# Performance work log

Hardware: AMD Instinct MI355X
Metric: run time of the kernel (lower is better)

The kernel has to match this reference:

```python
import jax, jax.numpy as jnp
import numpy as np

D_MODEL = 1024
H = 16
D_K = D_MODEL // H
B, S = 4, 2048


def setup_inputs() -> dict:
    key = jax.random.key(0)
    ks = jax.random.split(key, 12)
    s = 1.0 / np.sqrt(D_MODEL)
    inp = {
        "q": jax.random.normal(ks[0], (B, S, D_MODEL), jnp.float32),
        "k": jax.random.normal(ks[1], (B, S, D_MODEL), jnp.float32),
        "v": jax.random.normal(ks[2], (B, S, D_MODEL), jnp.float32),
        "mask": jax.random.randint(ks[3], (1, 1, S, S), 0, 2, jnp.int32),
        # torch nn.Linear convention: weight [out, in], y = x @ W.T + b
        "w_q": jax.random.uniform(ks[4], (D_MODEL, D_MODEL), jnp.float32, -s, s),
        "b_q": jax.random.uniform(ks[5], (D_MODEL,), jnp.float32, -s, s),
        "w_k": jax.random.uniform(ks[6], (D_MODEL, D_MODEL), jnp.float32, -s, s),
        "b_k": jax.random.uniform(ks[7], (D_MODEL,), jnp.float32, -s, s),
        "w_v": jax.random.uniform(ks[8], (D_MODEL, D_MODEL), jnp.float32, -s, s),
        "b_v": jax.random.uniform(ks[9], (D_MODEL,), jnp.float32, -s, s),
        "w_o": jax.random.uniform(ks[10], (D_MODEL, D_MODEL), jnp.float32, -s, s),
        "b_o": jax.random.uniform(ks[11], (D_MODEL,), jnp.float32, -s, s),
    }
    return inp


def _split_heads(x):
    b, s, _ = x.shape
    return x.reshape(b, s, H, D_K).transpose(0, 2, 1, 3)  # [B,H,S,Dk]


def reference(q, k, v, mask, w_q, b_q, w_k, b_k, w_v, b_v, w_o, b_o):
    query = _split_heads(q @ w_q.T + b_q)
    key = _split_heads(k @ w_k.T + b_k)
    value = _split_heads(v @ w_v.T + b_v)
    scores = jnp.einsum("bhqd,bhkd->bhqk", query, key) / jnp.sqrt(
        jnp.asarray(D_K, query.dtype))
    scores = jnp.where(mask == 0, jnp.asarray(-1e9, scores.dtype), scores)
    attn = jax.nn.softmax(scores, axis=-1)  # dropout p=0 (eval) -> identity
    x = jnp.einsum("bhqk,bhkd->bhqd", attn, value)
    x = x.transpose(0, 2, 1, 3).reshape(q.shape[0], -1, H * D_K)
    return x @ w_o.T + b_o
```

## Files before the change

### kernel.cpp

```cpp
#include <hip/hip_runtime.h>

typedef __bf16 bf16_t;
typedef __bf16 bf16x4 __attribute__((ext_vector_type(4)));
typedef __bf16 bf16x8 __attribute__((ext_vector_type(8)));
typedef float f32x4 __attribute__((ext_vector_type(4)));
typedef float f32x16 __attribute__((ext_vector_type(16)));
typedef unsigned int uint;
typedef uint uint2v __attribute__((ext_vector_type(2)));
typedef uint uint4v __attribute__((ext_vector_type(4)));

#define CSCALE 0.18033688011112042f

static __device__ __forceinline__ bf16_t f2bf(float f) {
  unsigned u = __builtin_bit_cast(unsigned, f);
  u = (u + 0x7fff + ((u >> 16) & 1)) >> 16;
  unsigned short h = (unsigned short)u;
  return __builtin_bit_cast(bf16_t, h);
}
static __device__ __forceinline__ uint cvt_pk(float a, float b) {
  uint r;
  asm("v_cvt_pk_bf16_f32 %0, %1, %2" : "=v"(r) : "v"(a), "v"(b));
  return r;
}

#define GLD_LDS(g, l) \
  __builtin_amdgcn_global_load_lds((const __attribute__((address_space(1))) void*)(g), \
                                   (__attribute__((address_space(3))) void*)(l), 16, 0, 0)
#define VMCNT(n) asm volatile("s_waitcnt vmcnt(" #n ")" ::: "memory")
#define LGKM0() asm volatile("s_waitcnt lgkmcnt(0)" ::: "memory")
#define BARRIER() do { __builtin_amdgcn_s_barrier(); __builtin_amdgcn_sched_barrier(0); } while (0)

__global__ void cvt4_f2b(const float* __restrict__ a, const float* __restrict__ b,
                         const float* __restrict__ c, const float* __restrict__ d,
                         bf16_t* __restrict__ oa, bf16_t* __restrict__ ob,
                         bf16_t* __restrict__ oc, bf16_t* __restrict__ od) {
  int i = blockIdx.x * 256 + threadIdx.x;
  const float* src = a;
  bf16_t* dst = oa;
  int w = i >> 18;
  i &= 262143;
  if (w == 1) { src = b; dst = ob; }
  else if (w == 2) { src = c; dst = oc; }
  else if (w == 3) { src = d; dst = od; }
  const float4 f = reinterpret_cast<const float4*>(src)[i];
  bf16x4 o;
  o[0] = f2bf(f.x); o[1] = f2bf(f.y); o[2] = f2bf(f.z); o[3] = f2bf(f.w);
  reinterpret_cast<bf16x4*>(dst)[i] = o;
}

__global__ void mask_bits_k(const int* __restrict__ m, uint* __restrict__ out) {
  int i = blockIdx.x * 256 + threadIdx.x;
  int q = i & 2047, t = i >> 11;
  const int* mrow = m + (size_t)q * 2048 + t * 32;
  uint bits = 0;
#pragma unroll
  for (int j = 0; j < 16; ++j) {
    int r0 = (j & 3) + 8 * (j >> 2);
    bits |= (mrow[r0] ? 1u : 0u) << j;
    bits |= (mrow[r0 + 4] ? 1u : 0u) << (16 + j);
  }
  out[(size_t)t * 2048 + q] = bits;
}

__global__ __launch_bounds__(256, 2) void qkv_gemm(
    const float* __restrict__ qA, const float* __restrict__ kA, const float* __restrict__ vA,
    const bf16_t* __restrict__ wq, const bf16_t* __restrict__ wk, const bf16_t* __restrict__ wv,
    const float* __restrict__ bq, const float* __restrict__ bk, const float* __restrict__ bv,
    bf16_t* __restrict__ Qp, bf16_t* __restrict__ Kp, bf16_t* __restrict__ Vt) {
  constexpr int K = 1024;
  __shared__ __align__(16) bf16_t AsB[2][128 * 32];
  __shared__ __align__(16) bf16_t BsB[3][256 * 32];
  const int z = blockIdx.z;
  const float* A = (z == 0) ? qA : (z == 1) ? kA : vA;
  const bf16_t* W = (z == 0) ? wq : (z == 1) ? wk : wv;
  const float* bias = (z == 0) ? bq : (z == 1) ? bk : bv;

  const int tid = threadIdx.x;
  const int lane = tid & 63;
  const int wv_ = tid >> 6;
  const int wm = (wv_ & 1) * 64, wn = (wv_ >> 1) * 128;
  const int l15 = lane & 15, lhi = lane >> 4;
  const int bm = blockIdx.x, bn = blockIdx.y;

  const int arow0 = tid >> 3;
  const int acol = tid & 7;
  const float* gA = A + (size_t)(bm * 128 + arow0) * K + acol * 4;
  const int brows = tid >> 2;
  const bf16_t* gB = W + (size_t)(bn * 256 + brows) * K + ((tid & 3) ^ (brows & 3)) * 8;

  f32x4 acc[4][8] = {};
  f32x4 rA0[4], rA1[4];

  auto A_LOAD = [&](int t, f32x4* R) {
#pragma unroll
    for (int L = 0; L < 4; ++L)
      R[L] = *reinterpret_cast<const f32x4*>(gA + (size_t)L * 32 * K + t * 32);
  };
  auto A_WRITE = [&](const f32x4* R, int buf) {
#pragma unroll
    for (int L = 0; L < 4; ++L) {
      int row = arow0 + L * 32;
      uint2v u;
      u[0] = cvt_pk(R[L][0], R[L][1]);
      u[1] = cvt_pk(R[L][2], R[L][3]);
      char* p = (char*)&AsB[buf][0] + row * 64 + (((acol >> 1) ^ (row & 3)) * 16) + (acol & 1) * 8;
      *reinterpret_cast<uint2v*>(p) = u;
    }
  };
  auto B_STAGE = [&](int t, int buf) {
#pragma unroll
    for (int c2 = 0; c2 < 4; ++c2)
      GLD_LDS(gB + (size_t)c2 * 64 * K + t * 32, (char*)&BsB[buf][0] + c2 * 4096 + wv_ * 1024);
  };
  auto COMPUTE = [&](int ba, int bb) {
    bf16x8 af[4], bfv[8];
#pragma unroll
    for (int i = 0; i < 4; ++i) {
      int arow = wm + i * 16 + l15;
      af[i] = *reinterpret_cast<const bf16x8*>(
          (const char*)&AsB[ba][0] + arow * 64 + ((lhi ^ (arow & 3)) * 16));
    }
#pragma unroll
    for (int j = 0; j < 8; ++j) {
      int br = wn + j * 16 + l15;
      bfv[j] = *reinterpret_cast<const bf16x8*>(
          (const char*)&BsB[bb][0] + br * 64 + ((lhi ^ (br & 3)) * 16));
    }
#pragma unroll
    for (int i = 0; i < 4; ++i)
#pragma unroll
      for (int j = 0; j < 8; ++j)
        acc[i][j] = __builtin_amdgcn_mfma_f32_16x16x32_bf16(af[i], bfv[j], acc[i][j], 0, 0, 0);
  };

#define QSTEP(T, RL, RW, BAW, BAC, BBC, BBS) \
  A_LOAD((T) + 2, RL); B_STAGE((T) + 2, BBS); \
  COMPUTE(BAC, BBC); \
  VMCNT(8); \
  A_WRITE(RW, BAW); \
  LGKM0(); BARRIER();

  A_LOAD(0, rA0); B_STAGE(0, 0);
  A_LOAD(1, rA1); B_STAGE(1, 1);
  VMCNT(8);
  A_WRITE(rA0, 0);
  LGKM0(); BARRIER();

#pragma unroll 1
  for (int t6 = 0; t6 < 30; t6 += 6) {
    QSTEP(t6 + 0, rA0, rA1, 1, 0, 0, 2)
    QSTEP(t6 + 1, rA1, rA0, 0, 1, 1, 0)
    QSTEP(t6 + 2, rA0, rA1, 1, 0, 2, 1)
    QSTEP(t6 + 3, rA1, rA0, 0, 1, 0, 2)
    QSTEP(t6 + 4, rA0, rA1, 1, 0, 1, 0)
    QSTEP(t6 + 5, rA1, rA0, 0, 1, 2, 1)
  }
  COMPUTE(0, 0);
  VMCNT(4);
  A_WRITE(rA1, 1);
  VMCNT(0);
  LGKM0(); BARRIER();
  COMPUTE(1, 1);

  if (z == 2) {
    const int b = (bm * 128) >> 11;
    const int s0 = (bm * 128) & 2047;
    bf16_t* vb = Vt + ((size_t)b * 1024 + bn * 256 + wn + l15) * 2048 + s0 + wm + lhi * 4;
#pragma unroll
    for (int j = 0; j < 8; ++j) {
      float bv2 = bias[bn * 256 + wn + j * 16 + l15];
#pragma unroll
      for (int i = 0; i < 4; ++i) {
        bf16x4 pk;
#pragma unroll
        for (int r = 0; r < 4; ++r) pk[r] = f2bf(acc[i][j][r] + bv2);
        *reinterpret_cast<bf16x4*>(vb + (size_t)(j * 16) * 2048 + i * 16) = pk;
      }
    }
  } else {
    bf16_t* O = (z == 0) ? Qp : Kp;
    const float scale = (z == 0) ? CSCALE : 1.0f;
#pragma unroll
    for (int i = 0; i < 4; ++i) {
#pragma unroll
      for (int j = 0; j < 8; ++j) {
        int n = bn * 256 + wn + j * 16 + l15;
        float bv2 = bias[n];
#pragma unroll
        for (int r = 0; r < 4; ++r) {
          int m = bm * 128 + wm + i * 16 + lhi * 4 + r;
          O[(size_t)m * 1024 + n] = f2bf((acc[i][j][r] + bv2) * scale);
        }
      }
    }
  }
#undef QSTEP
}

__global__ __launch_bounds__(256, 2) void gemm_o(
    const bf16_t* __restrict__ A, const bf16_t* __restrict__ Bw,
    const float* __restrict__ bias, float* __restrict__ Cout) {
  constexpr int K = 1024;
  __shared__ __align__(16) bf16_t As[3][128 * 32];
  __shared__ __align__(16) bf16_t Bs[3][256 * 32];
  const int tid = threadIdx.x;
  const int lane = tid & 63;
  const int wv_ = tid >> 6;
  const int wm = (wv_ & 1) * 64, wn = (wv_ >> 1) * 128;
  const int l15 = lane & 15, lhi = lane >> 4;
  const int bm = blockIdx.x, bn = blockIdx.y;
  const int rws = tid >> 2;
  const bf16_t* ga = A + (size_t)(bm * 128 + rws) * K + ((tid & 3) ^ (rws & 3)) * 8;
  const bf16_t* gb = Bw + (size_t)(bn * 256 + rws) * K + ((tid & 3) ^ (rws & 3)) * 8;
  f32x4 acc[4][8] = {};

  auto STAGE = [&](int t, int buf) {
#pragma unroll
    for (int c2 = 0; c2 < 2; ++c2)
      GLD_LDS(ga + (size_t)c2 * 64 * K + t * 32, (char*)&As[buf][0] + c2 * 4096 + wv_ * 1024);
#pragma unroll
    for (int c2 = 0; c2 < 4; ++c2)
      GLD_LDS(gb + (size_t)c2 * 64 * K + t * 32, (char*)&Bs[buf][0] + c2 * 4096 + wv_ * 1024);
  };
  auto COMPUTE = [&](int buf) {
    bf16x8 af[4], bfv[8];
#pragma unroll
    for (int i = 0; i < 4; ++i) {
      int arow = wm + i * 16 + l15;
      af[i] = *reinterpret_cast<const bf16x8*>(
          (const char*)&As[buf][0] + arow * 64 + ((lhi ^ (arow & 3)) * 16));
    }
#pragma unroll
    for (int j = 0; j < 8; ++j) {
      int br = wn + j * 16 + l15;
      bfv[j] = *reinterpret_cast<const bf16x8*>(
          (const char*)&Bs[buf][0] + br * 64 + ((lhi ^ (br & 3)) * 16));
    }
#pragma unroll
    for (int i = 0; i < 4; ++i)
#pragma unroll
      for (int j = 0; j < 8; ++j)
        acc[i][j] = __builtin_amdgcn_mfma_f32_16x16x32_bf16(af[i], bfv[j], acc[i][j], 0, 0, 0);
  };

  STAGE(0, 0);
  STAGE(1, 1);
#pragma unroll 1
  for (int tt = 0; tt < 30; tt += 3) {
    VMCNT(6); BARRIER(); COMPUTE(0); STAGE(tt + 2, 2);
    VMCNT(6); BARRIER(); COMPUTE(1); STAGE(tt + 3, 0);
    VMCNT(6); BARRIER(); COMPUTE(2); STAGE(tt + 4, 1);
  }
  VMCNT(6); BARRIER(); COMPUTE(0);
  VMCNT(0); BARRIER(); COMPUTE(1);

#pragma unroll
  for (int i = 0; i < 4; ++i)
#pragma unroll
    for (int j = 0; j < 8; ++j) {
      int n = bn * 256 + wn + j * 16 + l15;
      float bv2 = bias[n];
#pragma unroll
      for (int r = 0; r < 4; ++r) {
        int m = bm * 128 + wm + i * 16 + lhi * 4 + r;
        Cout[(size_t)m * 1024 + n] = acc[i][j][r] + bv2;
      }
    }
}

static __device__ __forceinline__ f32x16 qk_tile(const bf16_t* Kbuf, const bf16x8 qf[4],
                                                 int l31, int h) {
  f32x16 s = {};
  __builtin_amdgcn_s_setprio(1);
#pragma unroll
  for (int c = 0; c < 4; ++c) {
    bf16x8 kf = *reinterpret_cast<const bf16x8*>(Kbuf + l31 * 64 + ((h + 2 * c) ^ (l31 & 7)) * 8);
    s = __builtin_amdgcn_mfma_f32_32x32x16_bf16(kf, qf[c], s, 0, 0, 0);
  }
  __builtin_amdgcn_s_setprio(0);
  return s;
}

static __device__ __forceinline__ void softmax_tile(
    const f32x16& sv, uint mb, int h, f32x16& o0, f32x16& o1,
    float& mrun, float& lsum, bf16x8& pa0, bf16x8& pa1) {
  const uint mbh = mb >> (h << 4);
  float a0 = fmaxf(fmaxf(sv[0], sv[1]), sv[2]);
  float a1 = fmaxf(fmaxf(sv[3], sv[4]), sv[5]);
  float a2 = fmaxf(fmaxf(sv[6], sv[7]), sv[8]);
  float a3 = fmaxf(fmaxf(sv[9], sv[10]), sv[11]);
  float a4 = fmaxf(fmaxf(sv[12], sv[13]), sv[14]);
  float b0 = fmaxf(fmaxf(a0, a1), a2);
  float mt = fmaxf(fmaxf(b0, fmaxf(a3, a4)), sv[15]);
  if (!__all(mt - mrun <= 8.0f)) {
    float mtf = fmaxf(mt, __shfl_xor(mt, 32));
    float mnew = fmaxf(mrun, mtf);
    float alpha = __builtin_amdgcn_exp2f(mrun - mnew);
    lsum *= alpha;
#pragma unroll
    for (int r = 0; r < 16; ++r) {
      float ar = __shfl(alpha, (r & 3) + 8 * (r >> 2) + 4 * h);
      o0[r] *= ar; o1[r] *= ar;
    }
    mrun = mnew;
  }
  float p[16];
#pragma unroll
  for (int r = 0; r < 16; ++r) {
    float pv = __builtin_amdgcn_exp2f(sv[r] - mrun);
    uint smask = (uint)__builtin_amdgcn_sbfe((int)mbh, r, 1);
    p[r] = __builtin_bit_cast(float, __builtin_bit_cast(uint, pv) & smask);
  }
  float t0 = p[0] + p[1], t1 = p[2] + p[3], t2 = p[4] + p[5], t3 = p[6] + p[7];
  float t4 = p[8] + p[9], t5 = p[10] + p[11], t6 = p[12] + p[13], t7 = p[14] + p[15];
  t0 += t1; t2 += t3; t4 += t5; t6 += t7;
  lsum += (t0 + t2) + (t4 + t6);
  uint dw[8];
#pragma unroll
  for (int i = 0; i < 8; ++i) dw[i] = cvt_pk(p[2 * i], p[2 * i + 1]);
  uint e0 = (uint)__shfl_xor((int)(h ? dw[0] : dw[2]), 32);
  uint e1 = (uint)__shfl_xor((int)(h ? dw[1] : dw[3]), 32);
  uint e2 = (uint)__shfl_xor((int)(h ? dw[4] : dw[6]), 32);
  uint e3 = (uint)__shfl_xor((int)(h ? dw[5] : dw[7]), 32);
  uint4v ua0 = {h ? e0 : dw[0], h ? e1 : dw[1], h ? dw[2] : e0, h ? dw[3] : e1};
  uint4v ua1 = {h ? e2 : dw[4], h ? e3 : dw[5], h ? dw[6] : e2, h ? dw[7] : e3};
  pa0 = __builtin_bit_cast(bf16x8, ua0);
  pa1 = __builtin_bit_cast(bf16x8, ua1);
}

static __device__ __forceinline__ void pv_tile(const bf16_t* Vbuf, bf16x8 pa0, bf16x8 pa1,
                                               int l31, int h, f32x16& o0, f32x16& o1) {
  const int sw = l31 & 3;
  bf16x8 v00 = *reinterpret_cast<const bf16x8*>(Vbuf + l31 * 32 + ((h ^ sw) * 8));
  bf16x8 v01 = *reinterpret_cast<const bf16x8*>(Vbuf + l31 * 32 + (((2 + h) ^ sw) * 8));
  bf16x8 v10 = *reinterpret_cast<const bf16x8*>(Vbuf + (32 + l31) * 32 + ((h ^ sw) * 8));
  bf16x8 v11 = *reinterpret_cast<const bf16x8*>(Vbuf + (32 + l31) * 32 + (((2 + h) ^ sw) * 8));
  __builtin_amdgcn_s_setprio(1);
  o0 = __builtin_amdgcn_mfma_f32_32x32x16_bf16(pa0, v00, o0, 0, 0, 0);
  o0 = __builtin_amdgcn_mfma_f32_32x32x16_bf16(pa1, v01, o0, 0, 0, 0);
  o1 = __builtin_amdgcn_mfma_f32_32x32x16_bf16(pa0, v10, o1, 0, 0, 0);
  o1 = __builtin_amdgcn_mfma_f32_32x32x16_bf16(pa1, v11, o1, 0, 0, 0);
  __builtin_amdgcn_s_setprio(0);
}

__global__ __launch_bounds__(256, 4) void attn_kernel(
    const bf16_t* __restrict__ Qp, const bf16_t* __restrict__ Kp,
    const bf16_t* __restrict__ Vt, const uint* __restrict__ maskbits,
    bf16_t* __restrict__ Xb) {
  constexpr int S = 2048, D = 1024;
  __shared__ __align__(16) bf16_t Ks[2][32][64];
  __shared__ __align__(16) bf16_t Vs[2][64][32];
  const int tid = threadIdx.x;
  const int wv_ = tid >> 6, lane = tid & 63;
  const int l31 = lane & 31, h = lane >> 5;
  const int blk = blockIdx.x;
  const int bh = blk & 63, qt4 = blk >> 6;
  const int b = bh >> 4, hd = bh & 15;
  const int q0 = qt4 * 128 + wv_ * 32;

  const int rK = tid >> 3;
  const bf16_t* gK = Kp + ((size_t)b * S + rK) * D + hd * 64 + ((tid & 7) ^ (rK & 7)) * 8;
  const int rV = tid >> 2;
  const bf16_t* gV = Vt + ((size_t)b * 1024 + hd * 64 + rV) * (size_t)S + ((tid & 3) ^ (rV & 3)) * 8;
  char* ldsK0 = (char*)&Ks[0][0][0] + wv_ * 1024;
  char* ldsK1 = (char*)&Ks[1][0][0] + wv_ * 1024;
  char* ldsV0 = (char*)&Vs[0][0][0] + wv_ * 1024;
  char* ldsV1 = (char*)&Vs[1][0][0] + wv_ * 1024;

  const bf16_t* qbase = Qp + (size_t)(b * S + q0 + l31) * D + hd * 64 + h * 8;
  bf16x8 qf[4];
#pragma unroll
  for (int c = 0; c < 4; ++c)
    qf[c] = *reinterpret_cast<const bf16x8*>(qbase + 16 * c);

  const uint* mbase = maskbits + q0 + l31;

  f32x16 o0 = {}, o1 = {};
  float mrun = 0.f, lsum = 0.f;
  bf16x8 pa0, pa1;

  GLD_LDS(gK, ldsK0);
  GLD_LDS(gK + (size_t)32 * D, ldsK1);
  GLD_LDS(gV, ldsV0);
  uint mb0 = mbase[0];
  __syncthreads();
  {
    f32x16 s = qk_tile(&Ks[0][0][0], qf, l31, h);
    softmax_tile(s, mb0, h, o0, o1, mrun, lsum, pa0, pa1);
  }

  auto body = [&](int j, char* ldsK_st, char* ldsV_st, const bf16_t* Kq,
                  const bf16_t* Vp, bool stageK) {
    if (stageK) GLD_LDS(gK + (size_t)(j + 2) * 32 * D, ldsK_st);
    GLD_LDS(gV + (size_t)(j + 1) * 32, ldsV_st);
    uint mbn = mbase[(size_t)(j + 1) * 2048];
    f32x16 s = qk_tile(Kq, qf, l31, h);
    pv_tile(Vp, pa0, pa1, l31, h, o0, o1);
    softmax_tile(s, mbn, h, o0, o1, mrun, lsum, pa0, pa1);
    __syncthreads();
  };

#pragma unroll 1
  for (int jj = 0; jj < 31; ++jj) {
    const int j = 2 * jj;
    body(j,     ldsK0, ldsV1, &Ks[1][0][0], &Vs[0][0][0], true);
    body(j + 1, ldsK1, ldsV0, &Ks[0][0][0], &Vs[1][0][0], true);
  }
  body(62, ldsK0, ldsV1, &Ks[1][0][0], &Vs[0][0][0], false);
  pv_tile(&Vs[1][0][0], pa0, pa1, l31, h, o0, o1);

  lsum += __shfl_xor(lsum, 32);
  float linv = __builtin_amdgcn_rcpf(lsum);
  bf16_t* xrow = Xb + (size_t)(b * S + q0) * D + hd * 64 + l31;
#pragma unroll
  for (int r = 0; r < 16; ++r) {
    int qrow = (r & 3) + 8 * (r >> 2) + 4 * h;
    float lr = __shfl(linv, qrow);
    xrow[(size_t)qrow * D] = f2bf(o0[r] * lr);
    xrow[(size_t)qrow * D + 32] = f2bf(o1[r] * lr);
  }
}

extern "C" void kernel_launch(void* const* d_in, const int* in_sizes, int n_in,
                              void* d_out, int out_size, void* d_ws, size_t ws_size,
                              hipStream_t stream) {
  const float* q = (const float*)d_in[0];
  const float* k = (const float*)d_in[1];
  const float* v = (const float*)d_in[2];
  const int* mask = (const int*)d_in[3];
  const float* w_q = (const float*)d_in[4];
  const float* b_q = (const float*)d_in[5];
  const float* w_k = (const float*)d_in[6];
  const float* b_k = (const float*)d_in[7];
  const float* w_v = (const float*)d_in[8];
  const float* b_v = (const float*)d_in[9];
  const float* w_o = (const float*)d_in[10];
  const float* b_o = (const float*)d_in[11];

  char* ws = (char*)d_ws;
  const size_t SZ = (size_t)8192 * 1024 * 2;
  bf16_t* Qp = (bf16_t*)(ws + 0 * SZ);
  bf16_t* Kp = (bf16_t*)(ws + 1 * SZ);
  bf16_t* Vt = (bf16_t*)(ws + 2 * SZ);
  bf16_t* Xb = (bf16_t*)(ws + 3 * SZ);
  uint* maskB = (uint*)(ws + 4 * SZ);
  bf16_t* wqb = (bf16_t*)(ws + 4 * SZ + 8388608);
  bf16_t* wkb = wqb + 1048576;
  bf16_t* wvb = wkb + 1048576;
  bf16_t* wob = wvb + 1048576;

  cvt4_f2b<<<4096, 256, 0, stream>>>(w_q, w_k, w_v, w_o, wqb, wkb, wvb, wob);
  mask_bits_k<<<512, 256, 0, stream>>>(mask, maskB);

  dim3 g3(64, 4, 3);
  qkv_gemm<<<g3, 256, 0, stream>>>(q, k, v, wqb, wkb, wvb, b_q, b_k, b_v, Qp, Kp, Vt);
  attn_kernel<<<1024, 256, 0, stream>>>(Qp, Kp, Vt, maskB, Xb);
  gemm_o<<<dim3(64, 4), 256, 0, stream>>>(Xb, wob, b_o, (float*)d_out);
}
```

Measured before the change: 237.1 us.

## Stage K/V tiles through registers into padded LDS instead of direct global-to-LDS loads

```diff
diff --git a/kernel.cpp b/kernel.cpp
--- a/kernel.cpp
+++ b/kernel.cpp
@@ -274,7 +274,7 @@
   __builtin_amdgcn_s_setprio(1);
 #pragma unroll
   for (int c = 0; c < 4; ++c) {
-    bf16x8 kf = *reinterpret_cast<const bf16x8*>(Kbuf + l31 * 64 + ((h + 2 * c) ^ (l31 & 7)) * 8);
+    bf16x8 kf = *reinterpret_cast<const bf16x8*>(Kbuf + l31 * 72 + h * 8 + 16 * c);
     s = __builtin_amdgcn_mfma_f32_32x32x16_bf16(kf, qf[c], s, 0, 0, 0);
   }
   __builtin_amdgcn_s_setprio(0);
@@ -330,11 +330,10 @@
 
 static __device__ __forceinline__ void pv_tile(const bf16_t* Vbuf, bf16x8 pa0, bf16x8 pa1,
                                                int l31, int h, f32x16& o0, f32x16& o1) {
-  const int sw = l31 & 3;
-  bf16x8 v00 = *reinterpret_cast<const bf16x8*>(Vbuf + l31 * 32 + ((h ^ sw) * 8));
-  bf16x8 v01 = *reinterpret_cast<const bf16x8*>(Vbuf + l31 * 32 + (((2 + h) ^ sw) * 8));
-  bf16x8 v10 = *reinterpret_cast<const bf16x8*>(Vbuf + (32 + l31) * 32 + ((h ^ sw) * 8));
-  bf16x8 v11 = *reinterpret_cast<const bf16x8*>(Vbuf + (32 + l31) * 32 + (((2 + h) ^ sw) * 8));
+  bf16x8 v00 = *reinterpret_cast<const bf16x8*>(Vbuf + l31 * 40 + h * 8);
+  bf16x8 v01 = *reinterpret_cast<const bf16x8*>(Vbuf + l31 * 40 + 16 + h * 8);
+  bf16x8 v10 = *reinterpret_cast<const bf16x8*>(Vbuf + (32 + l31) * 40 + h * 8);
+  bf16x8 v11 = *reinterpret_cast<const bf16x8*>(Vbuf + (32 + l31) * 40 + 16 + h * 8);
   __builtin_amdgcn_s_setprio(1);
   o0 = __builtin_amdgcn_mfma_f32_32x32x16_bf16(pa0, v00, o0, 0, 0, 0);
   o0 = __builtin_amdgcn_mfma_f32_32x32x16_bf16(pa1, v01, o0, 0, 0, 0);
@@ -348,8 +347,8 @@
     const bf16_t* __restrict__ Vt, const uint* __restrict__ maskbits,
     bf16_t* __restrict__ Xb) {
   constexpr int S = 2048, D = 1024;
-  __shared__ __align__(16) bf16_t Ks[2][32][64];
-  __shared__ __align__(16) bf16_t Vs[2][64][32];
+  __shared__ __align__(16) bf16_t Ks[2][32][72];
+  __shared__ __align__(16) bf16_t Vs[2][64][40];
   const int tid = threadIdx.x;
   const int wv_ = tid >> 6, lane = tid & 63;
   const int l31 = lane & 31, h = lane >> 5;
@@ -358,14 +357,14 @@
   const int b = bh >> 4, hd = bh & 15;
   const int q0 = qt4 * 128 + wv_ * 32;
 
-  const int rK = tid >> 3;
-  const bf16_t* gK = Kp + ((size_t)b * S + rK) * D + hd * 64 + ((tid & 7) ^ (rK & 7)) * 8;
-  const int rV = tid >> 2;
-  const bf16_t* gV = Vt + ((size_t)b * 1024 + hd * 64 + rV) * (size_t)S + ((tid & 3) ^ (rV & 3)) * 8;
-  char* ldsK0 = (char*)&Ks[0][0][0] + wv_ * 1024;
-  char* ldsK1 = (char*)&Ks[1][0][0] + wv_ * 1024;
-  char* ldsV0 = (char*)&Vs[0][0][0] + wv_ * 1024;
-  char* ldsV1 = (char*)&Vs[1][0][0] + wv_ * 1024;
+  const int rK = tid >> 3, sK = tid & 7;
+  const int rV = tid >> 2, sV = tid & 3;
+  const bf16_t* gK = Kp + ((size_t)b * S + rK) * D + hd * 64 + sK * 8;
+  const bf16_t* gV = Vt + ((size_t)b * 1024 + hd * 64 + rV) * (size_t)S + sV * 8;
+  bf16_t* wK0 = &Ks[0][rK][sK * 8];
+  bf16_t* wK1 = &Ks[1][rK][sK * 8];
+  bf16_t* wV0 = &Vs[0][rV][sV * 8];
+  bf16_t* wV1 = &Vs[1][rV][sV * 8];
 
   const bf16_t* qbase = Qp + (size_t)(b * S + q0 + l31) * D + hd * 64 + h * 8;
   bf16x8 qf[4];
@@ -379,9 +378,14 @@
   float mrun = 0.f, lsum = 0.f;
   bf16x8 pa0, pa1;
 
-  GLD_LDS(gK, ldsK0);
-  GLD_LDS(gK + (size_t)32 * D, ldsK1);
-  GLD_LDS(gV, ldsV0);
+  {
+    bf16x8 k0 = *reinterpret_cast<const bf16x8*>(gK);
+    bf16x8 k1 = *reinterpret_cast<const bf16x8*>(gK + (size_t)32 * D);
+    bf16x8 v0 = *reinterpret_cast<const bf16x8*>(gV);
+    *reinterpret_cast<bf16x8*>(wK0) = k0;
+    *reinterpret_cast<bf16x8*>(wK1) = k1;
+    *reinterpret_cast<bf16x8*>(wV0) = v0;
+  }
   uint mb0 = mbase[0];
   __syncthreads();
   {
@@ -389,24 +393,27 @@
     softmax_tile(s, mb0, h, o0, o1, mrun, lsum, pa0, pa1);
   }
 
-  auto body = [&](int j, char* ldsK_st, char* ldsV_st, const bf16_t* Kq,
+  auto body = [&](int j, bf16_t* wK_st, bf16_t* wV_st, const bf16_t* Kq,
                   const bf16_t* Vp, bool stageK) {
-    if (stageK) GLD_LDS(gK + (size_t)(j + 2) * 32 * D, ldsK_st);
-    GLD_LDS(gV + (size_t)(j + 1) * 32, ldsV_st);
+    bf16x8 kreg, vreg;
+    if (stageK) kreg = *reinterpret_cast<const bf16x8*>(gK + (size_t)(j + 2) * 32 * D);
+    vreg = *reinterpret_cast<const bf16x8*>(gV + (size_t)(j + 1) * 32);
     uint mbn = mbase[(size_t)(j + 1) * 2048];
     f32x16 s = qk_tile(Kq, qf, l31, h);
     pv_tile(Vp, pa0, pa1, l31, h, o0, o1);
     softmax_tile(s, mbn, h, o0, o1, mrun, lsum, pa0, pa1);
+    if (stageK) *reinterpret_cast<bf16x8*>(wK_st) = kreg;
+    *reinterpret_cast<bf16x8*>(wV_st) = vreg;
     __syncthreads();
   };
 
 #pragma unroll 1
   for (int jj = 0; jj < 31; ++jj) {
     const int j = 2 * jj;
-    body(j,     ldsK0, ldsV1, &Ks[1][0][0], &Vs[0][0][0], true);
-    body(j + 1, ldsK1, ldsV0, &Ks[0][0][0], &Vs[1][0][0], true);
-  }
-  body(62, ldsK0, ldsV1, &Ks[1][0][0], &Vs[0][0][0], false);
+    body(j,     wK0, wV1, &Ks[1][0][0], &Vs[0][0][0], true);
+    body(j + 1, wK1, wV0, &Ks[0][0][0], &Vs[1][0][0], true);
+  }
+  body(62, wK0, wV1, &Ks[1][0][0], &Vs[0][0][0], false);
   pv_tile(&Vs[1][0][0], pa0, pa1, l31, h, o0, o1);
 
   lsum += __shfl_xor(lsum, 32);
```

Result: no change. 237.9 us (+0.3%).
